# Optimization experiments

Hardware: AMD Instinct MI355X
Metric: run time of the kernel (lower is better)

The kernel has to match this reference:

```python
import jax, jax.numpy as jnp
import numpy as np

THRESHOLD = 0.003  # pool_type[3]
EPS = 1e-7


def setup_inputs() -> dict:
    key = jax.random.key(0)
    k1, k2, k3, k4 = jax.random.split(key, 4)
    B, N, C = 64, 600, 256
    x = jax.random.normal(k1, (B, N, C), dtype=jnp.float32)
    A = jax.random.uniform(k2, (B, N, N), dtype=jnp.float32)
    mask = jax.random.bernoulli(k3, 0.9, (B, N))
    # small-scale projection weight so exp(scores) stays well-conditioned
    W = jax.random.normal(k4, (1, C), dtype=jnp.float32) * 0.05
    return {"x": x, "A": A, "mask": mask, "W": W}


def reference(x, A, mask, W):
    B, N, C = x.shape
    mf = mask.astype(x.dtype)
    # proj(x) -> (B,N,1) -> (B,N); alpha_pre = exp(.) masked
    scores = jnp.einsum('bnc,oc->bn', x, W)
    alpha_pre = jnp.exp(scores) * mf
    alpha = alpha_pre / (jnp.sum(alpha_pre, axis=1, keepdims=True) + EPS)
    x = x * alpha[..., None]
    # threshold masking
    mask = mask & (alpha > THRESHOLD)
    # drop_nodes_edges: topk over mask values + gather-compaction of x and A.
    # Static K=N (JIT-safe); equivalent to torch's dynamic N_nodes_max up to
    # trailing zero padding (padded rows/cols are fully masked out below).
    mvals, idx = jax.lax.top_k(mask.astype(jnp.int32), N)  # (B,N)
    mask_k = mvals.astype(bool)
    x = jnp.take_along_axis(x, idx[..., None], axis=1)          # (B,N,C)
    A = jnp.take_along_axis(A, idx[..., None], axis=1)          # rows
    A = jnp.take_along_axis(A, idx[:, None, :], axis=2)         # cols
    mask_matrix = mask_k[:, :, None] & mask_k[:, None, :]
    A = A * mask_matrix.astype(A.dtype)
    return x, A, mask_k
```

## Files before the change

### kernel.cpp

```cpp
#include <hip/hip_runtime.h>

#define B_DIM 64
#define N_NODES 600
#define C_DIM 256

constexpr float kThr = 0.003f;
constexpr float kEps = 1e-7f;

__global__ void k_scores(const float* __restrict__ x,
                         const float* __restrict__ W,
                         const int* __restrict__ mask,
                         float* __restrict__ alpha_pre) {
  const int row  = blockIdx.x * 4 + (threadIdx.x >> 6);
  const int lane = threadIdx.x & 63;
  const float4 xv = reinterpret_cast<const float4*>(x + (size_t)row * C_DIM)[lane];
  const float4 wv = reinterpret_cast<const float4*>(W)[lane];
  float s = xv.x * wv.x + xv.y * wv.y + xv.z * wv.z + xv.w * wv.w;
  #pragma unroll
  for (int off = 32; off > 0; off >>= 1) s += __shfl_down(s, off, 64);
  if (lane == 0) {
    const float ap = (mask[row] != 0) ? expf(s) : 0.0f;
    alpha_pre[row] = ap;
  }
}

__global__ void k_compact(const int* __restrict__ mask,
                          float* __restrict__ alpha,
                          int* __restrict__ idx,
                          int* __restrict__ Kbuf,
                          float* __restrict__ mask_out) {
  const int b = blockIdx.x;
  const int t = threadIdx.x;

  __shared__ float fs[1024];
  __shared__ int   sbuf[2][1024];

  const float ap = (t < N_NODES) ? alpha[b * N_NODES + t] : 0.0f;

  fs[t] = ap;
  __syncthreads();
  #pragma unroll
  for (int off = 512; off > 0; off >>= 1) {
    if (t < off) fs[t] += fs[t + off];
    __syncthreads();
  }
  const float S = fs[0];

  const float a = ap / (S + kEps);
  const int   m = (t < N_NODES) ? mask[b * N_NODES + t] : 0;
  const int keep = (m != 0 && a > kThr) ? 1 : 0;
  if (t < N_NODES) alpha[b * N_NODES + t] = a;

  int pin = 0;
  sbuf[0][t] = keep;
  __syncthreads();
  #pragma unroll
  for (int off = 1; off < 1024; off <<= 1) {
    int v = sbuf[pin][t];
    if (t >= off) v += sbuf[pin][t - off];
    sbuf[pin ^ 1][t] = v;
    pin ^= 1;
    __syncthreads();
  }
  const int incl = sbuf[pin][t];
  const int K    = sbuf[pin][1023];

  if (t < N_NODES) {
    const int pos = keep ? (incl - 1) : (K + (t - incl));
    idx[b * N_NODES + pos] = t;
    mask_out[b * N_NODES + t] = (t < K) ? 1.0f : 0.0f;
    if (t == 0) Kbuf[b] = K;
  }
}

__global__ void k_gather_x(const float* __restrict__ x,
                           const float* __restrict__ alpha,
                           const int* __restrict__ idx,
                           float* __restrict__ xo) {
  const int row  = blockIdx.x * 4 + (threadIdx.x >> 6);
  const int lane = threadIdx.x & 63;
  const int b = row / N_NODES;
  const int src = idx[row];
  const float a = alpha[b * N_NODES + src];
  float4 v = reinterpret_cast<const float4*>(
      x + ((size_t)b * N_NODES + src) * C_DIM)[lane];
  v.x *= a; v.y *= a; v.z *= a; v.w *= a;
  reinterpret_cast<float4*>(xo + (size_t)row * C_DIM)[lane] = v;
}

#define TILE_I 8
__global__ void k_gather_A(const float* __restrict__ A,
                           const int* __restrict__ idx,
                           const int* __restrict__ Kbuf,
                           float* __restrict__ Ao) {
  __shared__ int sidx[N_NODES];
  const int bi = blockIdx.x;
  const int b  = bi / (N_NODES / TILE_I);
  const int i0 = (bi % (N_NODES / TILE_I)) * TILE_I;
  const int t  = threadIdx.x;

  for (int j = t; j < N_NODES; j += 256) sidx[j] = idx[b * N_NODES + j];
  __syncthreads();
  const int K = Kbuf[b];

  const float* Ab  = A  + (size_t)b * N_NODES * N_NODES;
  float*       Aob = Ao + (size_t)b * N_NODES * N_NODES;

  #pragma unroll
  for (int ii = 0; ii < TILE_I; ++ii) {
    const int i = i0 + ii;
    float* Aorow = Aob + (size_t)i * N_NODES;
    if (i < K) {
      const float* Arow = Ab + (size_t)sidx[i] * N_NODES;
      for (int j = t; j < N_NODES; j += 256)
        Aorow[j] = (j < K) ? Arow[sidx[j]] : 0.0f;
    } else {
      for (int j = t; j < N_NODES; j += 256) Aorow[j] = 0.0f;
    }
  }
}

extern "C" void kernel_launch(void* const* d_in, const int* in_sizes, int n_in,
                              void* d_out, int out_size, void* d_ws, size_t ws_size,
                              hipStream_t stream) {
  const float* x    = (const float*)d_in[0];
  const float* A    = (const float*)d_in[1];
  const int*   mask = (const int*)d_in[2];
  const float* W    = (const float*)d_in[3];

  const size_t BN = (size_t)B_DIM * N_NODES;

  float* xo = (float*)d_out;
  float* Ao = xo + BN * C_DIM;
  float* mo = Ao + BN * N_NODES;

  float* alpha = (float*)d_ws;
  int*   idx   = (int*)(alpha + BN);
  int*   Kbuf  = idx + BN;

  k_scores<<<(int)(BN / 4), 256, 0, stream>>>(x, W, mask, alpha);
  k_compact<<<B_DIM, 1024, 0, stream>>>(mask, alpha, idx, Kbuf, mo);
  k_gather_x<<<(int)(BN / 4), 256, 0, stream>>>(x, alpha, idx, xo);
  k_gather_A<<<B_DIM * (N_NODES / TILE_I), 256, 0, stream>>>(A, idx, Kbuf, Ao);
}
```

Baseline: 49.34 us.

## Fuse scoring with compaction and x/A gathers into two kernels

Merges the score computation into the per-batch compaction kernel, so each batch is handled by one 1024-thread block that reads its x rows directly. The shared-memory Hillis-Steele scan is replaced by a wave-level shuffle scan plus per-wave totals. The two gather kernels become one launch that picks the x or A path by block index. The A path uses one wave per row and float4 stores. Launches drop from four to two, but scoring now runs on only 64 blocks, which may limit bandwidth on the first pass over x.

```diff
diff --git a/kernel.cpp b/kernel.cpp
--- a/kernel.cpp
+++ b/kernel.cpp
@@ -3,40 +3,48 @@
 #define B_DIM 64
 #define N_NODES 600
 #define C_DIM 256
+#define NV4 (N_NODES / 4)
+#define XROWS (B_DIM * N_NODES)
+#define XBLOCKS (XROWS / 4)
+#define A_ROWTILE 16
+#define ABLK_PER_B ((N_NODES + A_ROWTILE - 1) / A_ROWTILE)
+#define ABLOCKS (B_DIM * ABLK_PER_B)
 
 constexpr float kThr = 0.003f;
 constexpr float kEps = 1e-7f;
 
-__global__ void k_scores(const float* __restrict__ x,
-                         const float* __restrict__ W,
-                         const int* __restrict__ mask,
-                         float* __restrict__ alpha_pre) {
-  const int row  = blockIdx.x * 4 + (threadIdx.x >> 6);
-  const int lane = threadIdx.x & 63;
-  const float4 xv = reinterpret_cast<const float4*>(x + (size_t)row * C_DIM)[lane];
+__global__ __launch_bounds__(1024)
+void k_score_compact(const float* __restrict__ x,
+                     const float* __restrict__ W,
+                     const int* __restrict__ mask,
+                     float* __restrict__ alpha,
+                     int* __restrict__ idx,
+                     int* __restrict__ Kbuf,
+                     float* __restrict__ mask_out) {
+  const int b    = blockIdx.x;
+  const int t    = threadIdx.x;
+  const int wave = t >> 6;
+  const int lane = t & 63;
+
+  __shared__ float sAP[N_NODES];
+  __shared__ float fs[1024];
+  __shared__ int   wtot[16];
+
   const float4 wv = reinterpret_cast<const float4*>(W)[lane];
-  float s = xv.x * wv.x + xv.y * wv.y + xv.z * wv.z + xv.w * wv.w;
-  #pragma unroll
-  for (int off = 32; off > 0; off >>= 1) s += __shfl_down(s, off, 64);
-  if (lane == 0) {
-    const float ap = (mask[row] != 0) ? expf(s) : 0.0f;
-    alpha_pre[row] = ap;
+  const float* xb = x + (size_t)b * N_NODES * C_DIM;
+
+  for (int r = wave; r < N_NODES; r += 16) {
+    const float4 xv =
+        reinterpret_cast<const float4*>(xb + (size_t)r * C_DIM)[lane];
+    float s = xv.x * wv.x + xv.y * wv.y + xv.z * wv.z + xv.w * wv.w;
+    #pragma unroll
+    for (int off = 32; off > 0; off >>= 1) s += __shfl_down(s, off, 64);
+    if (lane == 0)
+      sAP[r] = (mask[b * N_NODES + r] != 0) ? expf(s) : 0.0f;
   }
-}
+  __syncthreads();
 
-__global__ void k_compact(const int* __restrict__ mask,
-                          float* __restrict__ alpha,
-                          int* __restrict__ idx,
-                          int* __restrict__ Kbuf,
-                          float* __restrict__ mask_out) {
-  const int b = blockIdx.x;
-  const int t = threadIdx.x;
-
-  __shared__ float fs[1024];
-  __shared__ int   sbuf[2][1024];
-
-  const float ap = (t < N_NODES) ? alpha[b * N_NODES + t] : 0.0f;
-
+  const float ap = (t < N_NODES) ? sAP[t] : 0.0f;
   fs[t] = ap;
   __syncthreads();
   #pragma unroll
@@ -47,75 +55,89 @@
   const float S = fs[0];
 
   const float a = ap / (S + kEps);
-  const int   m = (t < N_NODES) ? mask[b * N_NODES + t] : 0;
-  const int keep = (m != 0 && a > kThr) ? 1 : 0;
-  if (t < N_NODES) alpha[b * N_NODES + t] = a;
+  const int keep = (t < N_NODES && a > kThr) ? 1 : 0;
 
-  int pin = 0;
-  sbuf[0][t] = keep;
+  int incl = keep;
+  #pragma unroll
+  for (int off = 1; off < 64; off <<= 1) {
+    int v = __shfl_up(incl, off, 64);
+    if (lane >= off) incl += v;
+  }
+  if (lane == 63) wtot[wave] = incl;
   __syncthreads();
+  int offtot = 0, Ktot = 0;
   #pragma unroll
-  for (int off = 1; off < 1024; off <<= 1) {
-    int v = sbuf[pin][t];
-    if (t >= off) v += sbuf[pin][t - off];
-    sbuf[pin ^ 1][t] = v;
-    pin ^= 1;
-    __syncthreads();
+  for (int w2 = 0; w2 < 16; ++w2) {
+    const int v = wtot[w2];
+    if (w2 < wave) offtot += v;
+    Ktot += v;
   }
-  const int incl = sbuf[pin][t];
-  const int K    = sbuf[pin][1023];
+  incl += offtot;
+  const int K = Ktot;
 
   if (t < N_NODES) {
     const int pos = keep ? (incl - 1) : (K + (t - incl));
-    idx[b * N_NODES + pos] = t;
-    mask_out[b * N_NODES + t] = (t < K) ? 1.0f : 0.0f;
+    idx[b * N_NODES + pos]      = t;
+    alpha[b * N_NODES + t]      = a;
+    mask_out[b * N_NODES + t]   = (t < K) ? 1.0f : 0.0f;
     if (t == 0) Kbuf[b] = K;
   }
 }
 
-__global__ void k_gather_x(const float* __restrict__ x,
-                           const float* __restrict__ alpha,
-                           const int* __restrict__ idx,
-                           float* __restrict__ xo) {
-  const int row  = blockIdx.x * 4 + (threadIdx.x >> 6);
-  const int lane = threadIdx.x & 63;
-  const int b = row / N_NODES;
-  const int src = idx[row];
-  const float a = alpha[b * N_NODES + src];
-  float4 v = reinterpret_cast<const float4*>(
-      x + ((size_t)b * N_NODES + src) * C_DIM)[lane];
-  v.x *= a; v.y *= a; v.z *= a; v.w *= a;
-  reinterpret_cast<float4*>(xo + (size_t)row * C_DIM)[lane] = v;
-}
+__global__ __launch_bounds__(256)
+void k_gather(const float* __restrict__ x,
+              const float* __restrict__ A,
+              const float* __restrict__ alpha,
+              const int* __restrict__ idx,
+              const int* __restrict__ Kbuf,
+              float* __restrict__ xo,
+              float* __restrict__ Ao) {
+  const int bid  = blockIdx.x;
+  const int t    = threadIdx.x;
+  const int wave = t >> 6;
+  const int lane = t & 63;
 
-#define TILE_I 8
-__global__ void k_gather_A(const float* __restrict__ A,
-                           const int* __restrict__ idx,
-                           const int* __restrict__ Kbuf,
-                           float* __restrict__ Ao) {
-  __shared__ int sidx[N_NODES];
-  const int bi = blockIdx.x;
-  const int b  = bi / (N_NODES / TILE_I);
-  const int i0 = (bi % (N_NODES / TILE_I)) * TILE_I;
-  const int t  = threadIdx.x;
+  if (bid < XBLOCKS) {
+    const int row = bid * 4 + wave;
+    const int b   = row / N_NODES;
+    const int src = idx[row];
+    const float a = alpha[b * N_NODES + src];
+    float4 v = reinterpret_cast<const float4*>(
+        x + ((size_t)b * N_NODES + src) * C_DIM)[lane];
+    v.x *= a; v.y *= a; v.z *= a; v.w *= a;
+    reinterpret_cast<float4*>(xo + (size_t)row * C_DIM)[lane] = v;
+  } else {
+    const int abid = bid - XBLOCKS;
+    const int b    = abid / ABLK_PER_B;
+    const int i0   = (abid % ABLK_PER_B) * A_ROWTILE;
 
-  for (int j = t; j < N_NODES; j += 256) sidx[j] = idx[b * N_NODES + j];
-  __syncthreads();
-  const int K = Kbuf[b];
+    __shared__ int sidx[N_NODES];
+    const int K = Kbuf[b];
+    for (int j = t; j < K; j += 256) sidx[j] = idx[b * N_NODES + j];
+    __syncthreads();
 
-  const float* Ab  = A  + (size_t)b * N_NODES * N_NODES;
-  float*       Aob = Ao + (size_t)b * N_NODES * N_NODES;
+    const float* Ab  = A  + (size_t)b * N_NODES * N_NODES;
+    float*       Aob = Ao + (size_t)b * N_NODES * N_NODES;
 
-  #pragma unroll
-  for (int ii = 0; ii < TILE_I; ++ii) {
-    const int i = i0 + ii;
-    float* Aorow = Aob + (size_t)i * N_NODES;
-    if (i < K) {
-      const float* Arow = Ab + (size_t)sidx[i] * N_NODES;
-      for (int j = t; j < N_NODES; j += 256)
-        Aorow[j] = (j < K) ? Arow[sidx[j]] : 0.0f;
-    } else {
-      for (int j = t; j < N_NODES; j += 256) Aorow[j] = 0.0f;
+    for (int ii = wave; ii < A_ROWTILE; ii += 4) {
+      const int i = i0 + ii;
+      if (i >= N_NODES) break;
+      float4* orow = reinterpret_cast<float4*>(Aob + (size_t)i * N_NODES);
+      if (i < K) {
+        const float* Arow = Ab + (size_t)sidx[i] * N_NODES;
+        for (int j4 = lane; j4 < NV4; j4 += 64) {
+          const int j = j4 * 4;
+          float4 v;
+          v.x = (j + 0 < K) ? Arow[sidx[j + 0]] : 0.0f;
+          v.y = (j + 1 < K) ? Arow[sidx[j + 1]] : 0.0f;
+          v.z = (j + 2 < K) ? Arow[sidx[j + 2]] : 0.0f;
+          v.w = (j + 3 < K) ? Arow[sidx[j + 3]] : 0.0f;
+          orow[j4] = v;
+        }
+      } else {
+        const float4 z = {0.0f, 0.0f, 0.0f, 0.0f};
+        for (int j4 = lane; j4 < NV4; j4 += 64) orow[j4] = z;
+      }
     }
   }
 }
@@ -138,8 +160,6 @@
   int*   idx   = (int*)(alpha + BN);
   int*   Kbuf  = idx + BN;
 
-  k_scores<<<(int)(BN / 4), 256, 0, stream>>>(x, W, mask, alpha);
-  k_compact<<<B_DIM, 1024, 0, stream>>>(mask, alpha, idx, Kbuf, mo);
-  k_gather_x<<<(int)(BN / 4), 256, 0, stream>>>(x, alpha, idx, xo);
-  k_gather_A<<<B_DIM * (N_NODES / TILE_I), 256, 0, stream>>>(A, idx, Kbuf, Ao);
+  k_score_compact<<<B_DIM, 1024, 0, stream>>>(x, W, mask, alpha, idx, Kbuf, mo);
+  k_gather<<<XBLOCKS + ABLOCKS, 256, 0, stream>>>(x, A, alpha, idx, Kbuf, xo, Ao);
 }
```

Result: slower. 64.30 us (+30.3%).
